# Kernel optimization log

Hardware: AMD Instinct MI355X
Metric: run time of the kernel (lower is better)

Reference implementation:

```python
import jax, jax.numpy as jnp
import numpy as np

N_NODES = 50000
N_EDGES = 800000
NUM_FEATURES = 256
HIDDEN = 128
NUM_CLASSES = 64


def gcn_conv(x, edge_index, W, b):
    """PyG-style GCNConv: out = D^-1/2 (A+I) D^-1/2 (x W) + b.

    edge_index[0] = source (j), edge_index[1] = target (i);
    messages flow source -> target and are summed at the target.
    """
    n = x.shape[0]
    loop = jnp.arange(n, dtype=edge_index.dtype)
    src = jnp.concatenate([edge_index[0], loop])  # [E+N]
    dst = jnp.concatenate([edge_index[1], loop])  # [E+N]

    h = x @ W  # [N, out_dim] — transform before propagate, as in PyG GCNConv

    deg = jax.ops.segment_sum(jnp.ones_like(dst, dtype=h.dtype), dst, num_segments=n)
    dinv = jnp.where(deg > 0, jax.lax.rsqrt(deg), 0.0)
    norm = dinv[src] * dinv[dst]  # [E+N]

    out = jax.ops.segment_sum(norm[:, None] * h[src], dst, num_segments=n)
    return out + b


def setup_inputs() -> dict:
    key = jax.random.key(0)
    k1, k2, k3, k4 = jax.random.split(key, 4)
    x = jax.random.normal(k1, (N_NODES, NUM_FEATURES), dtype=jnp.float32)
    edge_index = jax.random.randint(k2, (2, N_EDGES), 0, N_NODES, dtype=jnp.int64)
    # Glorot-style init for the two GCN layer weights, zero bias (PyG default)
    W1 = jax.random.normal(k3, (NUM_FEATURES, HIDDEN), dtype=jnp.float32) * (1.0 / np.sqrt(NUM_FEATURES))
    b1 = jnp.zeros((HIDDEN,), dtype=jnp.float32)
    W2 = jax.random.normal(k4, (HIDDEN, NUM_CLASSES), dtype=jnp.float32) * (1.0 / np.sqrt(HIDDEN))
    b2 = jnp.zeros((NUM_CLASSES,), dtype=jnp.float32)
    return {"x": x, "edge_index": edge_index, "W1": W1, "b1": b1, "W2": W2, "b2": b2}


def reference(x, edge_index, W1, b1, W2, b2):
    h = gcn_conv(x, edge_index, W1, b1)
    h = jax.nn.relu(h)
    # dropout(p=0.5, training=True): fixed key stands in for torch RNG
    keep = jax.random.bernoulli(jax.random.key(42), 0.5, h.shape)
    h = jnp.where(keep, h * 2.0, 0.0)
    out = gcn_conv(h, edge_index, W2, b2)
    return out
```

## Files before the change

### kernel.cpp

```cpp
#include <hip/hip_runtime.h>


typedef __attribute__((ext_vector_type(8))) short bf16x8;
typedef __attribute__((ext_vector_type(4))) float f32x4;
typedef __attribute__((ext_vector_type(8))) unsigned short us8;

__device__ __forceinline__ unsigned tf_rotl(unsigned x, int d) {
    return (x << d) | (x >> (32 - d));
}

__device__ __forceinline__ bool dropout_keep(unsigned flat_idx) {
    const unsigned K0 = 0u, K1 = 42u;
    const unsigned K2 = K0 ^ K1 ^ 0x1BD11BDAu;
    unsigned x0 = 0u, x1 = flat_idx;
    x0 += K0; x1 += K1;
#define TF_R(r) { x0 += x1; x1 = tf_rotl(x1, (r)); x1 ^= x0; }
    TF_R(13) TF_R(15) TF_R(26) TF_R(6)
    x0 += K1; x1 += K2 + 1u;
    TF_R(17) TF_R(29) TF_R(16) TF_R(24)
    x0 += K2; x1 += K0 + 2u;
    TF_R(13) TF_R(15) TF_R(26) TF_R(6)
    x0 += K0; x1 += K1 + 3u;
    TF_R(17) TF_R(29) TF_R(16) TF_R(24)
    x0 += K1; x1 += K2 + 4u;
    TF_R(13) TF_R(15) TF_R(26) TF_R(6)
    x0 += K2; x1 += K0 + 5u;
#undef TF_R
    return (((x0 ^ x1) >> 31) & 1u) == 0u;
}

__device__ __forceinline__ unsigned short bf16_rn(float x) {
    unsigned u = __float_as_uint(x);
    unsigned r = u + 0x7FFFu + ((u >> 16) & 1u);
    return (unsigned short)(r >> 16);
}
__device__ __forceinline__ void split_bf16(float x, unsigned short& h, unsigned short& l) {
    h = bf16_rn(x);
    float fh = __uint_as_float(((unsigned)h) << 16);
    l = bf16_rn(x - fh);
}
__device__ __forceinline__ void split4(float4 v, ushort4& h, ushort4& l) {
    unsigned short h0, h1, h2, h3, l0, l1, l2, l3;
    split_bf16(v.x, h0, l0); split_bf16(v.y, h1, l1);
    split_bf16(v.z, h2, l2); split_bf16(v.w, h3, l3);
    h = make_ushort4(h0, h1, h2, h3);
    l = make_ushort4(l0, l1, l2, l3);
}

__device__ __forceinline__ int ei_stride(const int* __restrict__ ei) {
    bool i64 = true;
#pragma unroll
    for (int k = 1; k <= 15; k += 2) i64 = i64 && (ei[k] == 0);
    return i64 ? 2 : 1;
}

__global__ void count_deg(const int* __restrict__ ei, unsigned* __restrict__ deg, int E) {
    int e = blockIdx.x * blockDim.x + threadIdx.x;
    if (e >= E) return;
    size_t st = ei_stride(ei);
    atomicAdd(&deg[ei[((size_t)E + e) * st]], 1u);
}

__global__ __launch_bounds__(256)
void scan_phase1(const unsigned* __restrict__ deg, unsigned* __restrict__ blockSums,
                 float* __restrict__ dinv, int N) {
    const int i = blockIdx.x * 256 + threadIdx.x;
    const int lane = threadIdx.x & 63, wave = threadIdx.x >> 6;
    unsigned v = 0;
    if (i < N) {
        unsigned d = deg[i];
        v = (d + 7u) & ~7u;
        dinv[i] = rsqrtf((float)(d + 1u));
    }
    unsigned s = v;
#pragma unroll
    for (int o = 32; o > 0; o >>= 1) s += __shfl_down(s, o, 64);
    __shared__ unsigned ws[4];
    if (lane == 0) ws[wave] = s;
    __syncthreads();
    if (threadIdx.x == 0)
        blockSums[blockIdx.x] = ws[0] + ws[1] + ws[2] + ws[3];
}

__global__ __launch_bounds__(1024)
void scan_phase2(unsigned* __restrict__ blockSums, int nb) {
    __shared__ unsigned s[1024];
    const int t = threadIdx.x;
    unsigned v = (t < nb) ? blockSums[t] : 0u;
    s[t] = v;
    __syncthreads();
    for (int off = 1; off < 1024; off <<= 1) {
        unsigned u = (t >= off) ? s[t - off] : 0u;
        __syncthreads();
        s[t] += u;
        __syncthreads();
    }
    if (t < nb) blockSums[t] = s[t] - v;
}

__global__ __launch_bounds__(256)
void scan_phase3(const unsigned* __restrict__ deg, const unsigned* __restrict__ blockSums,
                 unsigned* __restrict__ rowptr, int N) {
    const int i = blockIdx.x * 256 + threadIdx.x;
    const int t = threadIdx.x;
    unsigned v = 0;
    if (i < N) v = (deg[i] + 7u) & ~7u;
    __shared__ unsigned s[256];
    s[t] = v;
    __syncthreads();
    for (int off = 1; off < 256; off <<= 1) {
        unsigned u = (t >= off) ? s[t - off] : 0u;
        __syncthreads();
        s[t] += u;
        __syncthreads();
    }
    const unsigned incl = s[t];
    const unsigned off0 = blockSums[blockIdx.x];
    if (i < N) {
        rowptr[i] = off0 + incl - v;
        if (i == N - 1) rowptr[N] = off0 + incl;
    }
}

__global__ void fill_pad(int* __restrict__ csr, int total, int N) {
    int i = blockIdx.x * blockDim.x + threadIdx.x;
    if (i < total) csr[i] = N;
}

__global__ void fill_csr(const int* __restrict__ ei, const unsigned* __restrict__ rowptr,
                         unsigned* __restrict__ cursor, int* __restrict__ csr, int E) {
    int e = blockIdx.x * blockDim.x + threadIdx.x;
    if (e >= E) return;
    size_t st = ei_stride(ei);
    int s = ei[(size_t)e * st];
    int d = ei[((size_t)E + e) * st];
    unsigned pos = atomicAdd(&cursor[d], 1u);
    csr[rowptr[d] + pos] = s;
}

__global__ void split_wT(const float* __restrict__ W, unsigned short* __restrict__ wT_hi,
                         unsigned short* __restrict__ wT_lo, int K, int NOUT) {
    int idx = blockIdx.x * blockDim.x + threadIdx.x;
    if (idx >= K * NOUT) return;
    int k = idx / NOUT, n = idx % NOUT;
    unsigned short h, l;
    split_bf16(W[idx], h, l);
    wT_hi[(size_t)n * K + k] = h;
    wT_lo[(size_t)n * K + k] = l;
}

template <int K_, int NOUT_, bool SPLITA>
__global__ __launch_bounds__(256)
void gemm_mfma(const void* __restrict__ Xv, const unsigned short* __restrict__ wT_hi,
               const unsigned short* __restrict__ wT_lo, const float* __restrict__ scale,
               unsigned short* __restrict__ Yb, int nrows) {
    constexpr int BM = 64, BK = 32, NKT = K_ / BK;
    constexpr int CT = NOUT_ / 64;
    constexpr int LDW = BK + 8;
    constexpr int WPT = NOUT_ / 32;

    __shared__ __attribute__((aligned(16))) unsigned short xs_hi[BM][LDW];
    __shared__ __attribute__((aligned(16))) unsigned short xs_lo[SPLITA ? BM : 1][SPLITA ? LDW : 1];
    __shared__ __attribute__((aligned(16))) unsigned short ws_hi[NOUT_][LDW];
    __shared__ __attribute__((aligned(16))) unsigned short ws_lo[NOUT_][LDW];

    const int t = threadIdx.x;
    const int wave = t >> 6, lane = t & 63;
    const int m16 = lane & 15, kg = lane >> 4;
    const int row0 = blockIdx.x * BM;
    const int n0 = wave * (16 * CT);

    if (blockIdx.x == 0 && t < NOUT_ / 8) {
        us8 z = (us8)0;
        *(us8*)&Yb[(size_t)nrows * NOUT_ + t * 8] = z;
    }

    const float* Xf = (const float*)Xv;
    const unsigned short* Xb = (const unsigned short*)Xv;

    f32x4 acc[4][CT];
#pragma unroll
    for (int r = 0; r < 4; ++r)
#pragma unroll
        for (int c = 0; c < CT; ++c) acc[r][c] = {0.f, 0.f, 0.f, 0.f};

    float4 xpre[2];
    us8 xpre_b;
    ushort4 wpre_h[WPT], wpre_l[WPT];

    if constexpr (SPLITA) {
#pragma unroll
        for (int i = 0; i < 2; ++i) {
            int idx = t + i * 256;
            int r = idx >> 3, c4 = idx & 7;
            int gr = row0 + r;
            xpre[i] = (gr < nrows) ? *(const float4*)&Xf[(size_t)gr * K_ + c4 * 4]
                                   : make_float4(0.f, 0.f, 0.f, 0.f);
        }
    } else {
        int r = t >> 2, c8 = t & 3;
        int gr = row0 + r;
        xpre_b = (gr < nrows) ? *(const us8*)&Xb[(size_t)gr * K_ + c8 * 8] : (us8)0;
    }
#pragma unroll
    for (int i = 0; i < WPT; ++i) {
        int idx = t + i * 256;
        int n = idx >> 3, c4 = idx & 7;
        wpre_h[i] = *(const ushort4*)&wT_hi[(size_t)n * K_ + c4 * 4];
        wpre_l[i] = *(const ushort4*)&wT_lo[(size_t)n * K_ + c4 * 4];
    }

    for (int kb = 0; kb < NKT; ++kb) {
        if constexpr (SPLITA) {
#pragma unroll
            for (int i = 0; i < 2; ++i) {
                int idx = t + i * 256;
                int r = idx >> 3, c4 = idx & 7;
                ushort4 h, l;
                split4(xpre[i], h, l);
                *(ushort4*)&xs_hi[r][c4 * 4] = h;
                *(ushort4*)&xs_lo[r][c4 * 4] = l;
            }
        } else {
            int r = t >> 2, c8 = t & 3;
            *(us8*)&xs_hi[r][c8 * 8] = xpre_b;
        }
#pragma unroll
        for (int i = 0; i < WPT; ++i) {
            int idx = t + i * 256;
            int n = idx >> 3, c4 = idx & 7;
            *(ushort4*)&ws_hi[n][c4 * 4] = wpre_h[i];
            *(ushort4*)&ws_lo[n][c4 * 4] = wpre_l[i];
        }
        __syncthreads();

        if (kb + 1 < NKT) {
            const int koff = (kb + 1) * BK;
            if constexpr (SPLITA) {
#pragma unroll
                for (int i = 0; i < 2; ++i) {
                    int idx = t + i * 256;
                    int r = idx >> 3, c4 = idx & 7;
                    int gr = row0 + r;
                    xpre[i] = (gr < nrows) ? *(const float4*)&Xf[(size_t)gr * K_ + koff + c4 * 4]
                                           : make_float4(0.f, 0.f, 0.f, 0.f);
                }
            } else {
                int r = t >> 2, c8 = t & 3;
                int gr = row0 + r;
                xpre_b = (gr < nrows) ? *(const us8*)&Xb[(size_t)gr * K_ + koff + c8 * 8] : (us8)0;
            }
#pragma unroll
            for (int i = 0; i < WPT; ++i) {
                int idx = t + i * 256;
                int n = idx >> 3, c4 = idx & 7;
                wpre_h[i] = *(const ushort4*)&wT_hi[(size_t)n * K_ + koff + c4 * 4];
                wpre_l[i] = *(const ushort4*)&wT_lo[(size_t)n * K_ + koff + c4 * 4];
            }
        }

        bf16x8 bh[CT], bl[CT];
#pragma unroll
        for (int c = 0; c < CT; ++c) {
            bh[c] = *(const bf16x8*)&ws_hi[n0 + c * 16 + m16][kg * 8];
            bl[c] = *(const bf16x8*)&ws_lo[n0 + c * 16 + m16][kg * 8];
        }
#pragma unroll
        for (int r = 0; r < 4; ++r) {
            bf16x8 ah = *(const bf16x8*)&xs_hi[r * 16 + m16][kg * 8];
            if constexpr (SPLITA) {
                bf16x8 al = *(const bf16x8*)&xs_lo[r * 16 + m16][kg * 8];
#pragma unroll
                for (int c = 0; c < CT; ++c) {
                    acc[r][c] = __builtin_amdgcn_mfma_f32_16x16x32_bf16(ah, bh[c], acc[r][c], 0, 0, 0);
                    acc[r][c] = __builtin_amdgcn_mfma_f32_16x16x32_bf16(ah, bl[c], acc[r][c], 0, 0, 0);
                    acc[r][c] = __builtin_amdgcn_mfma_f32_16x16x32_bf16(al, bh[c], acc[r][c], 0, 0, 0);
                }
            } else {
#pragma unroll
                for (int c = 0; c < CT; ++c) {
                    acc[r][c] = __builtin_amdgcn_mfma_f32_16x16x32_bf16(ah, bh[c], acc[r][c], 0, 0, 0);
                    acc[r][c] = __builtin_amdgcn_mfma_f32_16x16x32_bf16(ah, bl[c], acc[r][c], 0, 0, 0);
                }
            }
        }
        __syncthreads();
    }

#pragma unroll
    for (int r = 0; r < 4; ++r) {
#pragma unroll
        for (int j = 0; j < 4; ++j) {
            int gr = row0 + r * 16 + kg * 4 + j;
            if (gr < nrows) {
                float s = scale[gr];
#pragma unroll
                for (int c = 0; c < CT; ++c)
                    Yb[(size_t)gr * NOUT_ + n0 + c * 16 + m16] = bf16_rn(acc[r][c][j] * s);
            }
        }
    }
}

__global__ __launch_bounds__(256)
void gather_drop(const unsigned* __restrict__ hs , const int* __restrict__ csr,
                 const unsigned* __restrict__ rowptr, const float* __restrict__ dinv,
                 const float* __restrict__ bias, unsigned* __restrict__ outb ,
                 int N) {
    const int node = blockIdx.x * 4 + (threadIdx.x >> 6);
    if (node >= N) return;
    const int lane = threadIdx.x & 63;
    const unsigned beg = rowptr[node];
    const unsigned end = rowptr[node + 1];
    const float dn = dinv[node];

    unsigned v = hs[(size_t)node * 64 + lane];
    float ax = __uint_as_float(v << 16);
    float ay = __uint_as_float(v & 0xffff0000u);
    for (unsigned k = beg; k < end; k += 8) {
        int j[8];
#pragma unroll
        for (int u = 0; u < 8; ++u) j[u] = csr[k + u];
        unsigned w[8];
#pragma unroll
        for (int u = 0; u < 8; ++u) w[u] = hs[(size_t)j[u] * 64 + lane];
#pragma unroll
        for (int u = 0; u < 8; ++u) {
            ax += __uint_as_float(w[u] << 16);
            ay += __uint_as_float(w[u] & 0xffff0000u);
        }
    }
    const int f0 = 2 * lane;
    float o0 = fmaxf(dn * ax + bias[f0], 0.0f);
    float o1 = fmaxf(dn * ay + bias[f0 + 1], 0.0f);
    unsigned base = (unsigned)node * 128u + (unsigned)f0;
    o0 = dropout_keep(base) ? 2.0f * o0 : 0.0f;
    o1 = dropout_keep(base + 1u) ? 2.0f * o1 : 0.0f;
    outb[(size_t)node * 64 + lane] =
        (unsigned)bf16_rn(o0) | ((unsigned)bf16_rn(o1) << 16);
}

__global__ __launch_bounds__(256)
void gather_out(const unsigned short* __restrict__ hs , const int* __restrict__ csr,
                const unsigned* __restrict__ rowptr, const float* __restrict__ dinv,
                const float* __restrict__ bias, float* __restrict__ outp, int N) {
    const int node = blockIdx.x * 4 + (threadIdx.x >> 6);
    if (node >= N) return;
    const int lane = threadIdx.x & 63;
    const unsigned beg = rowptr[node];
    const unsigned end = rowptr[node + 1];
    const float dn = dinv[node];

    float acc = __uint_as_float(((unsigned)hs[(size_t)node * 64 + lane]) << 16);
    for (unsigned k = beg; k < end; k += 8) {
        int j[8];
#pragma unroll
        for (int u = 0; u < 8; ++u) j[u] = csr[k + u];
        unsigned short w[8];
#pragma unroll
        for (int u = 0; u < 8; ++u) w[u] = hs[(size_t)j[u] * 64 + lane];
#pragma unroll
        for (int u = 0; u < 8; ++u) acc += __uint_as_float(((unsigned)w[u]) << 16);
    }
    outp[(size_t)node * 64 + lane] = dn * acc + bias[lane];
}

extern "C" void kernel_launch(void* const* d_in, const int* in_sizes, int n_in,
                              void* d_out, int out_size, void* d_ws, size_t ws_size,
                              hipStream_t stream) {
    const float* x  = (const float*)d_in[0];
    const int*   ei = (const int*)d_in[1];
    const float* W1 = (const float*)d_in[2];
    const float* b1 = (const float*)d_in[3];
    const float* W2 = (const float*)d_in[4];
    const float* b2 = (const float*)d_in[5];
    float* out = (float*)d_out;

    const int Fdim = 256, Hdim = 128, Cdim = 64;
    const int N = in_sizes[0] / Fdim;
    const int E = in_sizes[1] / 2;
    const int CSR_CAP = E + 7 * N;
    const int NB = (N + 255) / 256;

    unsigned short* wT1_hi = (unsigned short*)d_ws;
    unsigned short* wT1_lo = wT1_hi + 256 * 128;
    unsigned short* wT2_hi = wT1_lo + 256 * 128;
    unsigned short* wT2_lo = wT2_hi + 128 * 64;
    unsigned short* buffA  = wT2_lo + 128 * 64;
    unsigned short* buffB  = buffA + (size_t)(N + 1) * Hdim;
    unsigned* deg    = (unsigned*)(buffB + (size_t)N * Hdim);
    unsigned* cursor = deg + N;
    float*    dinv   = (float*)(cursor + N);
    unsigned* rowptr = (unsigned*)(dinv + N);
    unsigned* blockSums = rowptr + (N + 1);
    int*      csr    = (int*)(blockSums + NB);

    hipMemsetAsync(deg, 0, 2 * (size_t)N * sizeof(unsigned), stream);

    count_deg<<<(E + 255) / 256, 256, 0, stream>>>(ei, deg, E);
    fill_pad<<<(CSR_CAP + 255) / 256, 256, 0, stream>>>(csr, CSR_CAP, N);
    scan_phase1<<<NB, 256, 0, stream>>>(deg, blockSums, dinv, N);
    scan_phase2<<<1, 1024, 0, stream>>>(blockSums, NB);
    scan_phase3<<<NB, 256, 0, stream>>>(deg, blockSums, rowptr, N);
    fill_csr<<<(E + 255) / 256, 256, 0, stream>>>(ei, rowptr, cursor, csr, E);

    split_wT<<<(256 * 128 + 255) / 256, 256, 0, stream>>>(W1, wT1_hi, wT1_lo, 256, 128);
    split_wT<<<(128 * 64 + 255) / 256, 256, 0, stream>>>(W2, wT2_hi, wT2_lo, 128, 64);

    gemm_mfma<256, 128, true><<<(N + 63) / 64, 256, 0, stream>>>(x, wT1_hi, wT1_lo, dinv, buffA, N);
    gather_drop<<<(N + 3) / 4, 256, 0, stream>>>((const unsigned*)buffA, csr, rowptr, dinv, b1,
                                                 (unsigned*)buffB, N);

    gemm_mfma<128, 64, false><<<(N + 63) / 64, 256, 0, stream>>>(buffB, wT2_hi, wT2_lo, dinv, buffA, N);
    gather_out<<<(N + 3) / 4, 256, 0, stream>>>(buffA, csr, rowptr, dinv, b2, out, N);
}
```

Before: 288.2 us.

## Record edge slots during degree count and drop separate CSR fill passes

```diff
diff --git a/kernel.cpp b/kernel.cpp
--- a/kernel.cpp
+++ b/kernel.cpp
@@ -54,11 +54,12 @@
     return i64 ? 2 : 1;
 }
 
-__global__ void count_deg(const int* __restrict__ ei, unsigned* __restrict__ deg, int E) {
+__global__ void count_slot(const int* __restrict__ ei, unsigned* __restrict__ deg,
+                           unsigned* __restrict__ aux, int E) {
     int e = blockIdx.x * blockDim.x + threadIdx.x;
     if (e >= E) return;
     size_t st = ei_stride(ei);
-    atomicAdd(&deg[ei[((size_t)E + e) * st]], 1u);
+    aux[e] = atomicAdd(&deg[ei[((size_t)E + e) * st]], 1u);
 }
 
 __global__ __launch_bounds__(256)
@@ -100,11 +101,14 @@
 
 __global__ __launch_bounds__(256)
 void scan_phase3(const unsigned* __restrict__ deg, const unsigned* __restrict__ blockSums,
-                 unsigned* __restrict__ rowptr, int N) {
+                 unsigned* __restrict__ rowptr, int* __restrict__ csr, int N) {
     const int i = blockIdx.x * 256 + threadIdx.x;
     const int t = threadIdx.x;
-    unsigned v = 0;
-    if (i < N) v = (deg[i] + 7u) & ~7u;
+    unsigned d = 0, v = 0;
+    if (i < N) {
+        d = deg[i];
+        v = (d + 7u) & ~7u;
+    }
     __shared__ unsigned s[256];
     s[t] = v;
     __syncthreads();
@@ -117,36 +121,40 @@
     const unsigned incl = s[t];
     const unsigned off0 = blockSums[blockIdx.x];
     if (i < N) {
-        rowptr[i] = off0 + incl - v;
+        const unsigned rp = off0 + incl - v;
+        rowptr[i] = rp;
         if (i == N - 1) rowptr[N] = off0 + incl;
-    }
-}
-
-__global__ void fill_pad(int* __restrict__ csr, int total, int N) {
-    int i = blockIdx.x * blockDim.x + threadIdx.x;
-    if (i < total) csr[i] = N;
-}
-
-__global__ void fill_csr(const int* __restrict__ ei, const unsigned* __restrict__ rowptr,
-                         unsigned* __restrict__ cursor, int* __restrict__ csr, int E) {
+        for (unsigned u = d; u < v; ++u) csr[rp + u] = N;
+    }
+}
+
+__global__ void place_edges(const int* __restrict__ ei, const unsigned* __restrict__ rowptr,
+                            const unsigned* __restrict__ aux, int* __restrict__ csr, int E) {
     int e = blockIdx.x * blockDim.x + threadIdx.x;
     if (e >= E) return;
     size_t st = ei_stride(ei);
     int s = ei[(size_t)e * st];
     int d = ei[((size_t)E + e) * st];
-    unsigned pos = atomicAdd(&cursor[d], 1u);
-    csr[rowptr[d] + pos] = s;
-}
-
-__global__ void split_wT(const float* __restrict__ W, unsigned short* __restrict__ wT_hi,
-                         unsigned short* __restrict__ wT_lo, int K, int NOUT) {
+    csr[rowptr[d] + aux[e]] = s;
+}
+
+__global__ void split_both(const float* __restrict__ W1, const float* __restrict__ W2,
+                           unsigned short* __restrict__ wT1_hi, unsigned short* __restrict__ wT1_lo,
+                           unsigned short* __restrict__ wT2_hi, unsigned short* __restrict__ wT2_lo) {
     int idx = blockIdx.x * blockDim.x + threadIdx.x;
-    if (idx >= K * NOUT) return;
-    int k = idx / NOUT, n = idx % NOUT;
     unsigned short h, l;
-    split_bf16(W[idx], h, l);
-    wT_hi[(size_t)n * K + k] = h;
-    wT_lo[(size_t)n * K + k] = l;
+    if (idx < 256 * 128) {
+        int k = idx / 128, n = idx % 128;
+        split_bf16(W1[idx], h, l);
+        wT1_hi[(size_t)n * 256 + k] = h;
+        wT1_lo[(size_t)n * 256 + k] = l;
+    } else if (idx < 256 * 128 + 128 * 64) {
+        int j = idx - 256 * 128;
+        int k = j / 64, n = j % 64;
+        split_bf16(W2[j], h, l);
+        wT2_hi[(size_t)n * 128 + k] = h;
+        wT2_lo[(size_t)n * 128 + k] = l;
+    }
 }
 
 template <int K_, int NOUT_, bool SPLITA>
@@ -389,23 +397,22 @@
     unsigned short* buffA  = wT2_lo + 128 * 64;
     unsigned short* buffB  = buffA + (size_t)(N + 1) * Hdim;
     unsigned* deg    = (unsigned*)(buffB + (size_t)N * Hdim);
-    unsigned* cursor = deg + N;
-    float*    dinv   = (float*)(cursor + N);
+    float*    dinv   = (float*)(deg + N);
     unsigned* rowptr = (unsigned*)(dinv + N);
     unsigned* blockSums = rowptr + (N + 1);
-    int*      csr    = (int*)(blockSums + NB);
-
-    hipMemsetAsync(deg, 0, 2 * (size_t)N * sizeof(unsigned), stream);
-
-    count_deg<<<(E + 255) / 256, 256, 0, stream>>>(ei, deg, E);
-    fill_pad<<<(CSR_CAP + 255) / 256, 256, 0, stream>>>(csr, CSR_CAP, N);
+    unsigned* aux    = blockSums + NB;
+    int*      csr    = (int*)(aux + E);
+
+    hipMemsetAsync(deg, 0, (size_t)N * sizeof(unsigned), stream);
+
+    count_slot<<<(E + 255) / 256, 256, 0, stream>>>(ei, deg, aux, E);
     scan_phase1<<<NB, 256, 0, stream>>>(deg, blockSums, dinv, N);
     scan_phase2<<<1, 1024, 0, stream>>>(blockSums, NB);
-    scan_phase3<<<NB, 256, 0, stream>>>(deg, blockSums, rowptr, N);
-    fill_csr<<<(E + 255) / 256, 256, 0, stream>>>(ei, rowptr, cursor, csr, E);
-
-    split_wT<<<(256 * 128 + 255) / 256, 256, 0, stream>>>(W1, wT1_hi, wT1_lo, 256, 128);
-    split_wT<<<(128 * 64 + 255) / 256, 256, 0, stream>>>(W2, wT2_hi, wT2_lo, 128, 64);
+    scan_phase3<<<NB, 256, 0, stream>>>(deg, blockSums, rowptr, csr, N);
+    place_edges<<<(E + 255) / 256, 256, 0, stream>>>(ei, rowptr, aux, csr, E);
+
+    split_both<<<(256 * 128 + 128 * 64 + 255) / 256, 256, 0, stream>>>(
+        W1, W2, wT1_hi, wT1_lo, wT2_hi, wT2_lo);
 
     gemm_mfma<256, 128, true><<<(N + 63) / 64, 256, 0, stream>>>(x, wT1_hi, wT1_lo, dinv, buffA, N);
     gather_drop<<<(N + 3) / 4, 256, 0, stream>>>((const unsigned*)buffA, csr, rowptr, dinv, b1,
```

Result: faster. 246.8 us (-14.4%).
